# Optimization experiments

Measured on AMD Instinct MI355X. Metric: run time of the kernel, lower is better.

## Reference

```python
import jax, jax.numpy as jnp
from jax import lax
import numpy as np

T, B, D, N = 1024, 32, 1024, 64
INIT_D_ALPHA, INIT_ALPHA_BIAS = 0.1, 2.0

def _xavier(key, n_out, n_in):
    lim = float(np.sqrt(6.0 / (n_in + n_out)))
    return jax.random.uniform(key, (n_out, n_in), jnp.float32, -lim, lim)

def setup_inputs() -> dict:
    key = jax.random.key(0)
    k = jax.random.split(key, 5)
    return {
        "x": jax.random.normal(k[0], (T, B, D), jnp.float32),
        "S0": jnp.zeros((B, N, N), jnp.float32),
        "W_k": _xavier(k[1], N, D),
        "W_v": _xavier(k[2], N, D),
        "W_q": _xavier(k[3], N, D),
        "W_alpha": _xavier(k[4], N, D),
        "d_alpha": jnp.full((N,), INIT_D_ALPHA, jnp.float32),
        "b_alpha": jnp.full((N,), INIT_ALPHA_BIAS, jnp.float32),
    }

def reference(x, S0, W_k, W_v, W_q, W_alpha, d_alpha, b_alpha):
    # Precompute all per-step projections as batched GEMMs: [T,B,N]
    k = jnp.einsum('tbd,nd->tbn', x, W_k)
    v = jnp.einsum('tbd,nd->tbn', x, W_v)
    q = jnp.einsum('tbd,nd->tbn', x, W_q)
    ax = jnp.einsum('tbd,nd->tbn', x, W_alpha)

    def step(S, inp):
        k_t, v_t, q_t, ax_t = inp  # each [B,N]
        retrieved = jnp.einsum('bij,bj->bi', S, k_t)            # S @ k
        alpha = jax.nn.sigmoid(ax_t + d_alpha * retrieved + b_alpha)  # [B,N]
        outer = v_t[:, :, None] * k_t[:, None, :]               # outer(v,k) [B,N,N]
        S = alpha[:, :, None] * S + (1.0 - alpha)[:, :, None] * outer
        h = jnp.einsum('bij,bj->bi', S, q_t)                    # S @ q
        out = h * jax.nn.silu(h)                                # self-gated
        return S, out

    S_final, output = lax.scan(step, S0, (k, v, q, ax))
    return output, S_final
```

## Files before the change

kernel.cpp:

```cpp
#include <hip/hip_runtime.h>
#include <hip/hip_bf16.h>
#include <math.h>

#define T_STEPS 1024
#define BATCH   32
#define DIM     1024
#define NST     64
#define TBN     ((size_t)T_STEPS * BATCH * NST)

typedef __attribute__((ext_vector_type(8))) short bf16x8;
typedef __attribute__((ext_vector_type(4))) float f32x4;

#define NLOG2E (-1.44269504088896340736f)
#define MFMA16(a, b, c) __builtin_amdgcn_mfma_f32_16x16x32_bf16(a, b, c, 0, 0, 0)

__device__ unsigned short g_khi[TBN];
__device__ unsigned short g_klo[TBN];
__device__ unsigned short g_qhi[TBN];
__device__ unsigned short g_qlo[TBN];

__device__ __forceinline__ void gload16(const void* g, void* l)
{
    __builtin_amdgcn_global_load_lds(
        (const __attribute__((address_space(1))) unsigned int*)g,
        (__attribute__((address_space(3))) unsigned int*)l, 16, 0, 0);
}

__device__ __forceinline__ void split1_rne(float v, unsigned short& hi, unsigned short& lo)
{
    __hip_bfloat16 hb = __float2bfloat16(v);
    unsigned short hraw; __builtin_memcpy(&hraw, &hb, 2);
    float hf = __bfloat162float(hb);
    __hip_bfloat16 lb = __float2bfloat16(v - hf);
    unsigned short lraw; __builtin_memcpy(&lraw, &lb, 2);
    hi = hraw; lo = lraw;
}

__device__ __forceinline__ void cvt8(float4 v0, float4 v1, bf16x8& hi, bf16x8& lo)
{
    float f[8] = {v0.x, v0.y, v0.z, v0.w, v1.x, v1.y, v1.z, v1.w};
    bf16x8 h, l;
    #pragma unroll
    for (int i = 0; i < 8; i++) {
        unsigned short hr, lr;
        split1_rne(f[i], hr, lr);
        h[i] = (short)hr; l[i] = (short)lr;
    }
    hi = h; lo = l;
}


__global__ __launch_bounds__(256, 2)
void proj_gemm_v3(const float* __restrict__ x,
                  const float* __restrict__ Wk,
                  const float* __restrict__ Wv,
                  const float* __restrict__ Wq,
                  const float* __restrict__ Wa,
                  const float* __restrict__ b_alpha,
                  float* __restrict__ ws)
{
    __shared__ float As[2][128][32];
    __shared__ float Bs[2][128][32];

    const int tid  = threadIdx.x;
    const int lane = tid & 63;
    const int w    = tid >> 6;
    const int m0   = (blockIdx.x >> 1) * 128;
    const int nh   = blockIdx.x & 1;

    const int lrow  = lane >> 3;
    const int lgran = (lane & 7) ^ lrow;
    const float* ap[4];
    #pragma unroll
    for (int i = 0; i < 4; i++)
        ap[i] = x + (size_t)(m0 + 32*w + 8*i + lrow) * DIM + lgran * 4;
    const int proj = nh * 2 + (w >> 1);
    const float* Wsrc = (proj == 0) ? Wk : (proj == 1) ? Wv : (proj == 2) ? Wq : Wa;
    const float* bp[4];
    #pragma unroll
    for (int i = 0; i < 4; i++)
        bp[i] = Wsrc + (size_t)((w & 1)*32 + 8*i + lrow) * DIM + lgran * 4;

    auto stage = [&](int kb, int buf) {
        const int ko = kb * 32;
        #pragma unroll
        for (int i = 0; i < 4; i++) {
            gload16(ap[i] + ko, &As[buf][32*w + 8*i][0]);
            gload16(bp[i] + ko, &Bs[buf][32*w + 8*i][0]);
        }
    };

    const int fr = lane & 15;
    const int qi = lane >> 4;
    const int sx = fr & 7;
    const int mh  = w >> 1;
    const int nqh = w & 1;

    f32x4 acc[4][4];
    #pragma unroll
    for (int i = 0; i < 4; i++)
        #pragma unroll
        for (int j = 0; j < 4; j++)
            acc[i][j] = (f32x4)0.0f;

    stage(0, 0);
    __syncthreads();

    #pragma unroll 1
    for (int kb = 0; kb < 32; kb++) {
        const int buf = kb & 1;
        if (kb + 1 < 32) stage(kb + 1, buf ^ 1);

        bf16x8 ah[4], al[4], bh[4], bl[4];
        #pragma unroll
        for (int mt = 0; mt < 4; mt++) {
            const float* rp = &As[buf][mh*64 + mt*16 + fr][0];
            float4 v0 = *(const float4*)(rp + (((2*qi    ) ^ sx) * 4));
            float4 v1 = *(const float4*)(rp + (((2*qi + 1) ^ sx) * 4));
            cvt8(v0, v1, ah[mt], al[mt]);
        }
        #pragma unroll
        for (int nt = 0; nt < 4; nt++) {
            const float* rp = &Bs[buf][nqh*64 + nt*16 + fr][0];
            float4 v0 = *(const float4*)(rp + (((2*qi    ) ^ sx) * 4));
            float4 v1 = *(const float4*)(rp + (((2*qi + 1) ^ sx) * 4));
            cvt8(v0, v1, bh[nt], bl[nt]);
        }
        #pragma unroll
        for (int mt = 0; mt < 4; mt++)
            #pragma unroll
            for (int nt = 0; nt < 4; nt++) {
                acc[mt][nt] = MFMA16(ah[mt], bh[nt], acc[mt][nt]);
                acc[mt][nt] = MFMA16(al[mt], bh[nt], acc[mt][nt]);
                acc[mt][nt] = MFMA16(ah[mt], bl[nt], acc[mt][nt]);
            }

        __syncthreads();
    }

    const int nq = nh * 2 + nqh;
    float* outb = ws + (size_t)nq * TBN;
    const int r0 = qi * 4;
    float bav[4];
    #pragma unroll
    for (int nt = 0; nt < 4; nt++)
        bav[nt] = (nq == 3) ? b_alpha[nt*16 + fr] : 0.0f;
    const float scl = (nq == 3) ? NLOG2E : 1.0f;
    #pragma unroll
    for (int mt = 0; mt < 4; mt++)
        #pragma unroll
        for (int nt = 0; nt < 4; nt++)
            #pragma unroll
            for (int r = 0; r < 4; r++) {
                const float val = (acc[mt][nt][r] + bav[nt]) * scl;
                const size_t idx = (size_t)(m0 + mh*64 + mt*16 + r0 + r) * NST + nt*16 + fr;
                if (nq != 2)
                    outb[idx] = val;
                if (nq == 0 || nq == 2) {
                    unsigned short hr, lr;
                    split1_rne(val, hr, lr);
                    if (nq == 0) { g_khi[idx] = hr; g_klo[idx] = lr; }
                    else         { g_qhi[idx] = hr; g_qlo[idx] = lr; }
                }
            }
}


#define SCH 16
#define NCH (T_STEPS / SCH)

__global__ __launch_bounds__(256, 2)
void scan_gram2(const float* __restrict__ ws,
                const float* __restrict__ S0,
                const float* __restrict__ d_alpha,
                float* __restrict__ out)
{
    const float* kb_ = ws;
    const float* vb_ = ws + TBN;
    const float* ab_ = ws + 3 * TBN;

    __shared__ float k_st[2][SCH][64];
    __shared__ float va  [2][SCH][16];
    __shared__ float GG  [2][SCH][16][2];
    __shared__ unsigned short KH[2][SCH][64];
    __shared__ unsigned short KL[2][SCH][64];
    __shared__ unsigned short QH[2][SCH][64];
    __shared__ unsigned short QL[2][SCH][64];
    __shared__ float S_pvt[4][64];

    const int tid  = threadIdx.x;
    const int lane = tid & 63;
    const int w    = tid >> 6;
    const int bid  = blockIdx.x;
    const int b    = (bid & 7) * 4 + ((bid >> 3) & 3);
    const int rg   = bid >> 5;
    const int row  = rg * 4 + w;
    const int fr   = lane & 15;
    const int qi   = lane >> 4;

    const size_t stp = (size_t)BATCH * NST;

    float S = S0[((size_t)b * NST + row) * NST + lane];
    const float da_s = d_alpha[row] * NLOG2E;

    const float* ksrc = kb_ + (size_t)(4*w + qi) * stp + (size_t)b * NST + fr * 4;
    const float* vsrc = ((lane & 1) ? ab_ : vb_)
                      + (size_t)(lane >> 2) * stp + (size_t)b * NST + rg * 4;

    const unsigned short* pl_g = (w == 0) ? g_khi : (w == 1) ? g_klo
                               : (w == 2) ? g_qhi : g_qlo;
    const int prow  = lane >> 3;
    const int pgran = (lane & 7) ^ prow;
    const unsigned short* psrc0 = pl_g + ((size_t)prow       * stp + (size_t)b * NST + pgran * 8);
    const unsigned short* psrc1 = pl_g + ((size_t)(8 + prow) * stp + (size_t)b * NST + pgran * 8);

    auto stage = [&](int ch, int buf) {
        const size_t koff = (size_t)ch * SCH * stp;
        gload16(ksrc + koff, &k_st[buf][4*w][0]);
        if (w == 0)
            gload16(vsrc + koff, &va[buf][0][0]);
        unsigned short* pdst = (w == 0) ? &KH[buf][0][0] : (w == 1) ? &KL[buf][0][0]
                             : (w == 2) ? &QH[buf][0][0] : &QL[buf][0][0];
        gload16(psrc0 + koff, pdst);
        gload16(psrc1 + koff, pdst + 8 * 64);
    };

    const int c1 = (qi ^ (fr & 7)) * 8;
    const int c2 = c1 ^ 32;

    stage(0, 0);
    __syncthreads();

    float* op = out + (size_t)b * NST + row;
    float hv = 0.0f;

    #pragma unroll 1
    for (int ch = 0; ch < NCH; ch++) {
        const int buf = ch & 1;

        const bf16x8 Kh0 = *(const bf16x8*)&KH[buf][fr][c1];
        const bf16x8 Kh1 = *(const bf16x8*)&KH[buf][fr][c2];
        const bf16x8 Kl0 = *(const bf16x8*)&KL[buf][fr][c1];
        const bf16x8 Kl1 = *(const bf16x8*)&KL[buf][fr][c2];
        const bf16x8 Qh0 = *(const bf16x8*)&QH[buf][fr][c1];
        const bf16x8 Qh1 = *(const bf16x8*)&QH[buf][fr][c2];
        const bf16x8 Ql0 = *(const bf16x8*)&QL[buf][fr][c1];
        const bf16x8 Ql1 = *(const bf16x8*)&QL[buf][fr][c2];

        S_pvt[w][lane] = S;
        bf16x8 Sh0, Sl0, Sh1, Sl1;
        {
            float4 s0 = *(const float4*)&S_pvt[w][qi * 8];
            float4 s1 = *(const float4*)&S_pvt[w][qi * 8 + 4];
            cvt8(s0, s1, Sh0, Sl0);
            float4 s2 = *(const float4*)&S_pvt[w][32 + qi * 8];
            float4 s3 = *(const float4*)&S_pvt[w][32 + qi * 8 + 4];
            cvt8(s2, s3, Sh1, Sl1);
        }

        f32x4 aR0 = (f32x4)0.0f, aR1 = (f32x4)0.0f;
        f32x4 aH0 = (f32x4)0.0f, aH1 = (f32x4)0.0f;
        aR0 = MFMA16(Sh0, Kh0, aR0); aR0 = MFMA16(Sh0, Kl0, aR0); aR0 = MFMA16(Sl0, Kh0, aR0);
        aR1 = MFMA16(Sh1, Kh1, aR1); aR1 = MFMA16(Sh1, Kl1, aR1); aR1 = MFMA16(Sl1, Kh1, aR1);
        aH0 = MFMA16(Sh0, Qh0, aH0); aH0 = MFMA16(Sh0, Ql0, aH0); aH0 = MFMA16(Sl0, Qh0, aH0);
        aH1 = MFMA16(Sh1, Qh1, aH1); aH1 = MFMA16(Sh1, Ql1, aH1); aH1 = MFMA16(Sl1, Qh1, aH1);
        float R = aR0[0] + aR1[0];
        float H = aH0[0] + aH1[0];

        if (w == 0) {
            f32x4 aG = (f32x4)0.0f;
            aG = MFMA16(Kh0, Kh0, aG); aG = MFMA16(Kh0, Kl0, aG); aG = MFMA16(Kl0, Kh0, aG);
            aG = MFMA16(Kh1, Kh1, aG); aG = MFMA16(Kh1, Kl1, aG); aG = MFMA16(Kl1, Kh1, aG);
            #pragma unroll
            for (int r = 0; r < 4; r++) GG[buf][qi*4 + r][fr][0] = aG[r];
        } else if (w == 1) {
            f32x4 aQ = (f32x4)0.0f;
            aQ = MFMA16(Kh0, Qh0, aQ); aQ = MFMA16(Kh0, Ql0, aQ); aQ = MFMA16(Kl0, Qh0, aQ);
            aQ = MFMA16(Kh1, Qh1, aQ); aQ = MFMA16(Kh1, Ql1, aQ); aQ = MFMA16(Kl1, Qh1, aQ);
            #pragma unroll
            for (int r = 0; r < 4; r++) GG[buf][qi*4 + r][fr][1] = aQ[r];
        }

        __syncthreads();

        if (ch + 1 < NCH) stage(ch + 1, buf ^ 1);

        #pragma unroll
        for (int s = 0; s < SCH; s++) {
            const float  kcv = k_st[buf][s][lane];
            const float2 g2  = *(const float2*)&GG[buf][s][fr][0];
            const float  vv  = va[buf][s][w];
            const float  aa  = va[buf][s][4 + w];

            const float ret   = __int_as_float(
                __builtin_amdgcn_readlane(__float_as_int(R), s));
            const float z     = fmaf(da_s, ret, aa);
            const float e     = __builtin_amdgcn_exp2f(z);
            const float alpha = __builtin_amdgcn_rcpf(1.0f + e);
            const float bt    = (1.0f - alpha) * vv;

            R = fmaf(alpha, R, bt * g2.x);
            H = fmaf(alpha, H, bt * g2.y);
            S = fmaf(alpha, S, bt * kcv);

            hv = (lane == s) ? H : hv;
        }

        {
            const float sg = __builtin_amdgcn_rcpf(1.0f + __builtin_amdgcn_exp2f(hv * NLOG2E));
            const float o  = hv * hv * sg;
            if (lane < SCH)
                op[(size_t)(ch * SCH + lane) * stp] = o;
        }

        __syncthreads();
    }

    out[TBN + ((size_t)b * NST + row) * NST + lane] = S;
}


extern "C" void kernel_launch(void* const* d_in, const int* in_sizes, int n_in,
                              void* d_out, int out_size, void* d_ws, size_t ws_size,
                              hipStream_t stream)
{
    const float* x  = (const float*)d_in[0];
    const float* S0 = (const float*)d_in[1];
    const float* Wk = (const float*)d_in[2];
    const float* Wv = (const float*)d_in[3];
    const float* Wq = (const float*)d_in[4];
    const float* Wa = (const float*)d_in[5];
    const float* da = (const float*)d_in[6];
    const float* ba = (const float*)d_in[7];
    float* out = (float*)d_out;
    float* ws  = (float*)d_ws;

    proj_gemm_v3<<<dim3((T_STEPS * BATCH) / 128 * 2), 256, 0, stream>>>(x, Wk, Wv, Wq, Wa, ba, ws);

    scan_gram2<<<dim3(BATCH * 16), 256, 0, stream>>>(ws, S0, da, out);
}
```

Baseline: 356.2 us.

## Pre-split weights into bf16 hi/lo once and preload scan chunk operands

Adds a small kernel that splits the four projection weight matrices into bf16 high and low parts in global buffers. The GEMM then stages these bf16 tiles directly, so the fp32-to-bf16 split of B inside the inner loop goes away and the shared-memory footprint for B shrinks. The scan kernel also loads each chunk's LDS operands into registers before the serial recurrence loop, which shortens the dependent chain at the cost of more registers. The extra launch adds a little fixed overhead.

```diff
diff --git a/kernel.cpp b/kernel.cpp
--- a/kernel.cpp
+++ b/kernel.cpp
@@ -10,6 +10,7 @@
 
 typedef __attribute__((ext_vector_type(8))) short bf16x8;
 typedef __attribute__((ext_vector_type(4))) float f32x4;
+typedef __attribute__((ext_vector_type(4))) unsigned short u16x4;
 
 #define NLOG2E (-1.44269504088896340736f)
 #define MFMA16(a, b, c) __builtin_amdgcn_mfma_f32_16x16x32_bf16(a, b, c, 0, 0, 0)
@@ -18,6 +19,8 @@
 __device__ unsigned short g_klo[TBN];
 __device__ unsigned short g_qhi[TBN];
 __device__ unsigned short g_qlo[TBN];
+__device__ unsigned short g_whi[4 * 64 * 1024];
+__device__ unsigned short g_wlo[4 * 64 * 1024];
 
 __device__ __forceinline__ void gload16(const void* g, void* l)
 {
@@ -49,18 +52,41 @@
     hi = h; lo = l;
 }
 
+__global__ __launch_bounds__(256, 4)
+void split_w(const float* __restrict__ Wk, const float* __restrict__ Wv,
+             const float* __restrict__ Wq, const float* __restrict__ Wa)
+{
+    const int t = blockIdx.x * 256 + threadIdx.x;
+    const float* Ws[4] = {Wk, Wv, Wq, Wa};
+    #pragma unroll
+    for (int i = 0; i < 4; i++) {
+        const int f4  = i * 16384 + t;
+        const int idx = f4 * 4;
+        const int proj = idx >> 16;
+        const int rem  = idx & 65535;
+        const float4 v = *(const float4*)(Ws[proj] + rem);
+        const float f[4] = {v.x, v.y, v.z, v.w};
+        u16x4 h, l;
+        #pragma unroll
+        for (int j = 0; j < 4; j++) {
+            unsigned short hr, lr;
+            split1_rne(f[j], hr, lr);
+            h[j] = hr; l[j] = lr;
+        }
+        *(u16x4*)&g_whi[idx] = h;
+        *(u16x4*)&g_wlo[idx] = l;
+    }
+}
+
 
 __global__ __launch_bounds__(256, 2)
 void proj_gemm_v3(const float* __restrict__ x,
-                  const float* __restrict__ Wk,
-                  const float* __restrict__ Wv,
-                  const float* __restrict__ Wq,
-                  const float* __restrict__ Wa,
                   const float* __restrict__ b_alpha,
                   float* __restrict__ ws)
 {
     __shared__ float As[2][128][32];
-    __shared__ float Bs[2][128][32];
+    __shared__ unsigned short Bh[2][128][32];
+    __shared__ unsigned short Bl[2][128][32];
 
     const int tid  = threadIdx.x;
     const int lane = tid & 63;
@@ -74,19 +100,26 @@
     #pragma unroll
     for (int i = 0; i < 4; i++)
         ap[i] = x + (size_t)(m0 + 32*w + 8*i + lrow) * DIM + lgran * 4;
+
     const int proj = nh * 2 + (w >> 1);
-    const float* Wsrc = (proj == 0) ? Wk : (proj == 1) ? Wv : (proj == 2) ? Wq : Wa;
-    const float* bp[4];
-    #pragma unroll
-    for (int i = 0; i < 4; i++)
-        bp[i] = Wsrc + (size_t)((w & 1)*32 + 8*i + lrow) * DIM + lgran * 4;
+    const int brow0 = (w & 1) * 32 + (lane >> 2);
+    const int bcol  = (lane & 3) * 8;
+    const unsigned short* bsrc[2];
+    #pragma unroll
+    for (int j = 0; j < 2; j++)
+        bsrc[j] = (const unsigned short*)g_whi
+                + (size_t)proj * 65536 + (size_t)(brow0 + 16*j) * DIM + bcol;
+    const size_t lo_off = (size_t)(g_wlo - g_whi);
 
     auto stage = [&](int kb, int buf) {
         const int ko = kb * 32;
         #pragma unroll
-        for (int i = 0; i < 4; i++) {
+        for (int i = 0; i < 4; i++)
             gload16(ap[i] + ko, &As[buf][32*w + 8*i][0]);
-            gload16(bp[i] + ko, &Bs[buf][32*w + 8*i][0]);
+        #pragma unroll
+        for (int j = 0; j < 2; j++) {
+            gload16(bsrc[j] + ko,          &Bh[buf][32*w + 16*j][0]);
+            gload16(bsrc[j] + lo_off + ko, &Bl[buf][32*w + 16*j][0]);
         }
     };
 
@@ -121,10 +154,8 @@
         }
         #pragma unroll
         for (int nt = 0; nt < 4; nt++) {
-            const float* rp = &Bs[buf][nqh*64 + nt*16 + fr][0];
-            float4 v0 = *(const float4*)(rp + (((2*qi    ) ^ sx) * 4));
-            float4 v1 = *(const float4*)(rp + (((2*qi + 1) ^ sx) * 4));
-            cvt8(v0, v1, bh[nt], bl[nt]);
+            bh[nt] = *(const bf16x8*)&Bh[buf][nqh*64 + nt*16 + fr][qi * 8];
+            bl[nt] = *(const bf16x8*)&Bl[buf][nqh*64 + nt*16 + fr][qi * 8];
         }
         #pragma unroll
         for (int mt = 0; mt < 4; mt++)
@@ -285,23 +316,28 @@
 
         if (ch + 1 < NCH) stage(ch + 1, buf ^ 1);
 
+        float  kreg[SCH], vvr[SCH], aar[SCH];
+        float2 greg[SCH];
         #pragma unroll
         for (int s = 0; s < SCH; s++) {
-            const float  kcv = k_st[buf][s][lane];
-            const float2 g2  = *(const float2*)&GG[buf][s][fr][0];
-            const float  vv  = va[buf][s][w];
-            const float  aa  = va[buf][s][4 + w];
-
+            kreg[s] = k_st[buf][s][lane];
+            greg[s] = *(const float2*)&GG[buf][s][fr][0];
+            vvr[s]  = va[buf][s][w];
+            aar[s]  = va[buf][s][4 + w];
+        }
+
+        #pragma unroll
+        for (int s = 0; s < SCH; s++) {
             const float ret   = __int_as_float(
                 __builtin_amdgcn_readlane(__float_as_int(R), s));
-            const float z     = fmaf(da_s, ret, aa);
+            const float z     = fmaf(da_s, ret, aar[s]);
             const float e     = __builtin_amdgcn_exp2f(z);
             const float alpha = __builtin_amdgcn_rcpf(1.0f + e);
-            const float bt    = (1.0f - alpha) * vv;
-
-            R = fmaf(alpha, R, bt * g2.x);
-            H = fmaf(alpha, H, bt * g2.y);
-            S = fmaf(alpha, S, bt * kcv);
+            const float bt    = (1.0f - alpha) * vvr[s];
+
+            R = fmaf(alpha, R, bt * greg[s].x);
+            H = fmaf(alpha, H, bt * greg[s].y);
+            S = fmaf(alpha, S, bt * kreg[s]);
 
             hv = (lane == s) ? H : hv;
         }
@@ -335,7 +371,9 @@
     float* out = (float*)d_out;
     float* ws  = (float*)d_ws;
 
-    proj_gemm_v3<<<dim3((T_STEPS * BATCH) / 128 * 2), 256, 0, stream>>>(x, Wk, Wv, Wq, Wa, ba, ws);
+    split_w<<<dim3(64), 256, 0, stream>>>(Wk, Wv, Wq, Wa);
+
+    proj_gemm_v3<<<dim3((T_STEPS * BATCH) / 128 * 2), 256, 0, stream>>>(x, ba, ws);
 
     scan_gram2<<<dim3(BATCH * 16), 256, 0, stream>>>(ws, S0, da, out);
 }
```

After: 353.8 us. Within noise of the previous version (-0.7%).
